# Kernel tuning notes

Hardware: AMD Instinct MI355X
Metric: run time of the kernel (lower is better)

## Reference

```python
import jax, jax.numpy as jnp
import numpy as np

B, N = 4096, 64
H_DIM, U_DIM, Z_DIM, ATTN_DIM, RANK, ALPHA = 256, 128, 16, 64, 4, 1.0
SCALE = ALPHA / float(RANK)  # LowRankDelta scale
LN_EPS = 1e-5


def setup_inputs() -> dict:
    key = jax.random.key(0)
    ks = jax.random.split(key, 12)
    std = 0.02
    return {
        "h": jax.random.normal(ks[0], (B, N, H_DIM), jnp.float32),
        "u": jax.random.normal(ks[1], (B, N, U_DIM), jnp.float32),
        "z": jax.random.normal(ks[2], (B, N, Z_DIM), jnp.float32),
        # LowRankDelta weights (stored as [in, rank] / [rank, out]); up weights
        # are zero-init in torch but randomized here so the math is non-trivial.
        "qd_down": jax.random.normal(ks[3], (H_DIM + Z_DIM, RANK), jnp.float32) * std,
        "qd_up": jax.random.normal(ks[4], (RANK, ATTN_DIM), jnp.float32) * std,
        "kd_down": jax.random.normal(ks[5], (U_DIM, RANK), jnp.float32) * std,
        "kd_up": jax.random.normal(ks[6], (RANK, ATTN_DIM), jnp.float32) * std,
        "vd_down": jax.random.normal(ks[7], (U_DIM, RANK), jnp.float32) * std,
        "vd_up": jax.random.normal(ks[8], (RANK, ATTN_DIM), jnp.float32) * std,
        "od_down": jax.random.normal(ks[9], (ATTN_DIM, RANK), jnp.float32) * std,
        "od_up": jax.random.normal(ks[10], (RANK, U_DIM), jnp.float32) * std,
        # MemeticStateCell: mix_in = z+h+u = 400
        "ug_w": jax.random.normal(ks[11], (Z_DIM + H_DIM + U_DIM, Z_DIM), jnp.float32) * std,
        "ug_b": jnp.zeros((Z_DIM,), jnp.float32),
        "cand_w": jax.random.normal(jax.random.fold_in(key, 99), (Z_DIM + H_DIM + U_DIM, Z_DIM), jnp.float32) * std,
        "cand_b": jnp.zeros((Z_DIM,), jnp.float32),
        "eta_logit": jnp.float32(-1.5),
    }


def _layer_norm(x):
    mu = jnp.mean(x, axis=-1, keepdims=True)
    var = jnp.mean(jnp.square(x - mu), axis=-1, keepdims=True)
    return (x - mu) * jax.lax.rsqrt(var + LN_EPS)


def reference(h, u, z, qd_down, qd_up, kd_down, kd_up, vd_down, vd_up,
              od_down, od_up, ug_w, ug_b, cand_w, cand_b, eta_logit):
    # low-rank q/k/v deltas
    q_in = jnp.concatenate([h, z], axis=-1)                 # [B,N,H+Z]
    q = (q_in @ qd_down) @ qd_up * SCALE                    # [B,N,A]
    k = (u @ kd_down) @ kd_up * SCALE                       # [B,N,A]
    v = (u @ vd_down) @ vd_up * SCALE                       # [B,N,A]

    # masked self-attention over agents
    scores = jnp.einsum('bnd,bmd->bnm', q, k) / jnp.sqrt(jnp.float32(ATTN_DIM))
    eye = jnp.eye(scores.shape[-1], dtype=bool)             # self-mask
    scores = jnp.where(eye, -jnp.inf, scores)
    attn = jax.nn.softmax(scores, axis=-1)                  # [B,N,N]
    c_latent = jnp.einsum('bnm,bmd->bnd', attn, v)          # [B,N,A]
    c = (c_latent @ od_down) @ od_up * SCALE                # [B,N,U]

    # GRU-like gated memetic state update + layernorm
    mix = jnp.concatenate([z, h, c], axis=-1)               # [B,N,Z+H+U]
    gate = jax.nn.sigmoid(mix @ ug_w + ug_b)
    eta = jax.nn.sigmoid(eta_logit)
    proposal = jnp.tanh(mix @ cand_w + cand_b)
    eg = eta * gate
    z_next = _layer_norm((1.0 - eg) * z + eg * proposal)

    return (c, z_next, attn, q, k, v)
```

## Files before the change

### kernel.cpp

```cpp
#include <hip/hip_runtime.h>
#include <math.h>

typedef float v4f __attribute__((ext_vector_type(4)));
typedef short v8s __attribute__((ext_vector_type(8)));

#define NBATCH 4096
#define NT 64
#define HD 256
#define UD 128
#define ZD 16
#define AD 64
#define LRSCALE 0.25f

#define OFF_C    0UL
#define OFF_ZN   33554432UL
#define OFF_ATTN 37748736UL
#define OFF_Q    54525952UL
#define OFF_K    71303168UL
#define OFF_V    88080384UL

#define WS_WT2 13824
#define WS_WOT 15872
#define WS_WCT 24064
#define WS_TOTAL 28160

__device__ __forceinline__ short f2bf(float x) {
  unsigned u = __float_as_uint(x);
  u = (u + 0x7fffu + ((u >> 16) & 1u)) >> 16;
  return (short)u;
}
__device__ __forceinline__ v8s ld8(const short* p) { return *(const v8s*)p; }
__device__ __forceinline__ v8s pack8(v4f x0, v4f x1) {
  v8s a;
  a[0] = f2bf(x0.x); a[1] = f2bf(x0.y); a[2] = f2bf(x0.z); a[3] = f2bf(x0.w);
  a[4] = f2bf(x1.x); a[5] = f2bf(x1.y); a[6] = f2bf(x1.z); a[7] = f2bf(x1.w);
  return a;
}

__global__ void prep_weights(
    const float* __restrict__ qd_down, const float* __restrict__ kd_down,
    const float* __restrict__ vd_down, const float* __restrict__ od_down,
    const float* __restrict__ od_up, const float* __restrict__ ug_w,
    const float* __restrict__ cand_w, short* __restrict__ ws)
{
  int idx = blockIdx.x * 256 + threadIdx.x;
  if (idx < WS_WT2) {
    int n = idx / 288, k = idx - n * 288;
    float val = 0.f;
    if (n < 4) {
      if (k < 272) val = qd_down[k * 4 + n];
    } else if (n >= 16) {
      const float* W = (n < 32) ? ug_w : cand_w;
      int o = (n < 32) ? (n - 16) : (n - 32);
      if (k < 256) val = W[(16 + k) * 16 + o];
      else if (k < 272) val = W[(k - 256) * 16 + o];
    }
    ws[idx] = f2bf(val);
  } else if (idx < WS_WOT) {
    int j = idx - WS_WT2;
    int n = j >> 7, k = j & 127;
    float val = 0.f;
    if (n < 4) val = kd_down[k * 4 + n];
    else if (n < 8) val = vd_down[k * 4 + (n - 4)];
    ws[idx] = f2bf(val);
  } else if (idx < WS_WCT) {
    int j = idx - WS_WOT;
    int e2 = j >> 6, d = j & 63;
    float a = od_down[d * 4 + 0] * od_up[e2] + od_down[d * 4 + 1] * od_up[128 + e2]
            + od_down[d * 4 + 2] * od_up[256 + e2] + od_down[d * 4 + 3] * od_up[384 + e2];
    ws[idx] = f2bf(a * LRSCALE);
  } else if (idx < WS_TOTAL) {
    int j = idx - WS_WCT;
    int o = j >> 7, e2 = j & 127;
    const float* W = (o < 16) ? ug_w : cand_w;
    ws[idx] = f2bf(W[(272 + e2) * 16 + (o & 15)]);
  }
}

__global__ __launch_bounds__(256, 3)
void memetic_fused(
    const float* __restrict__ hg, const float* __restrict__ ug2,
    const float* __restrict__ zg,
    const float* __restrict__ qd_up, const float* __restrict__ kd_up,
    const float* __restrict__ vd_up,
    const float* __restrict__ ug_b, const float* __restrict__ cand_b,
    const float* __restrict__ eta_logit,
    const short* __restrict__ wsw,
    float* __restrict__ c_o, float* __restrict__ zn_o,
    float* __restrict__ attn_o, float* __restrict__ q_o,
    float* __restrict__ k_o, float* __restrict__ v_o)
{
  __shared__ float g1out[NT * 33];
  __shared__ float qkv4[NT * 13];
  __shared__ char scr[36864];

  const int b = blockIdx.x;
  const int tid = threadIdx.x;
  const int lane = tid & 63;
  const int wv = tid >> 6;
  const int quad = lane >> 4;
  const int l16 = lane & 15;

  const short* WT1g = wsw;
  const short* WT2g = wsw + WS_WT2;
  const short* WOTg = wsw + WS_WOT;
  const short* WCTg = wsw + WS_WCT;

  const int tok = wv * 16 + l16;
  const float* hrow = hg + ((size_t)b * NT + tok) * HD;
  const float* urow = ug2 + ((size_t)b * NT + tok) * UD;
  const float* zrow = zg + ((size_t)b * NT + tok) * ZD;

  v4f acc1[3];
  for (int i = 0; i < 3; ++i) acc1[i] = (v4f){0.f, 0.f, 0.f, 0.f};
#pragma unroll
  for (int kc = 0; kc < 9; ++kc) {
    v8s a;
    if (kc < 8) {
      v4f x0 = *(const v4f*)(hrow + kc * 32 + quad * 8);
      v4f x1 = *(const v4f*)(hrow + kc * 32 + quad * 8 + 4);
      a = pack8(x0, x1);
    } else if (quad < 2) {
      v4f x0 = *(const v4f*)(zrow + quad * 8);
      v4f x1 = *(const v4f*)(zrow + quad * 8 + 4);
      a = pack8(x0, x1);
    } else {
      a = (v8s){0, 0, 0, 0, 0, 0, 0, 0};
    }
    const short* wrow = WT1g + kc * 32 + quad * 8;
#pragma unroll
    for (int nt = 0; nt < 3; ++nt) {
      v8s bb = ld8(wrow + (nt * 16 + l16) * 288);
      acc1[nt] = __builtin_amdgcn_mfma_f32_16x16x32_bf16(a, bb, acc1[nt], 0, 0, 0);
    }
  }

  v4f acc2 = (v4f){0.f, 0.f, 0.f, 0.f};
#pragma unroll
  for (int kc = 0; kc < 4; ++kc) {
    v4f x0 = *(const v4f*)(urow + kc * 32 + quad * 8);
    v4f x1 = *(const v4f*)(urow + kc * 32 + quad * 8 + 4);
    v8s a = pack8(x0, x1);
    v8s bb = ld8(WT2g + l16 * 128 + kc * 32 + quad * 8);
    acc2 = __builtin_amdgcn_mfma_f32_16x16x32_bf16(a, bb, acc2, 0, 0, 0);
  }

  if (l16 < 4) {
#pragma unroll
    for (int r = 0; r < 4; ++r)
      qkv4[(wv * 16 + quad * 4 + r) * 13 + l16] = acc1[0][r];
  }
#pragma unroll
  for (int r = 0; r < 4; ++r) {
    int row = wv * 16 + quad * 4 + r;
    g1out[row * 33 + l16] = acc1[1][r];
    g1out[row * 33 + 16 + l16] = acc1[2][r];
  }
  if (l16 < 8) {
#pragma unroll
    for (int r = 0; r < 4; ++r)
      qkv4[(wv * 16 + quad * 4 + r) * 13 + 4 + l16] = acc2[r];
  }
  __syncthreads();

  {
    short* q_s = (short*)scr;
    short* k_s = (short*)(scr + 9216);
    short* vT = (short*)(scr + 18432);
    float qup[4], kup[4], vup[4];
#pragma unroll
    for (int r = 0; r < 4; ++r) {
      qup[r] = qd_up[r * AD + lane];
      kup[r] = kd_up[r * AD + lane];
      vup[r] = vd_up[r * AD + lane];
    }
    for (int i = 0; i < 16; ++i) {
      int t = wv * 16 + i;
      const float* p4 = qkv4 + t * 13;
      float qv = LRSCALE * (p4[0] * qup[0] + p4[1] * qup[1] + p4[2] * qup[2] + p4[3] * qup[3]);
      float kv = LRSCALE * (p4[4] * kup[0] + p4[5] * kup[1] + p4[6] * kup[2] + p4[7] * kup[3]);
      float vv = LRSCALE * (p4[8] * vup[0] + p4[9] * vup[1] + p4[10] * vup[2] + p4[11] * vup[3]);
      size_t go = ((size_t)b * NT + t) * AD + lane;
      q_o[go] = qv; k_o[go] = kv; v_o[go] = vv;
      q_s[t * 72 + lane] = f2bf(qv);
      k_s[t * 72 + lane] = f2bf(kv);
      vT[lane * 72 + t] = f2bf(vv);
    }
  }
  __syncthreads();

  v4f acc3[4];
  for (int i = 0; i < 4; ++i) acc3[i] = (v4f){0.f, 0.f, 0.f, 0.f};
  {
    short* q_s = (short*)scr;
    short* k_s = (short*)(scr + 9216);
#pragma unroll
    for (int kc = 0; kc < 2; ++kc) {
      v8s bb = ld8(k_s + (wv * 16 + l16) * 72 + kc * 32 + quad * 8);
#pragma unroll
      for (int mt = 0; mt < 4; ++mt) {
        v8s a = ld8(q_s + (mt * 16 + l16) * 72 + kc * 32 + quad * 8);
        acc3[mt] = __builtin_amdgcn_mfma_f32_16x16x32_bf16(a, bb, acc3[mt], 0, 0, 0);
      }
    }
  }
  __syncthreads();
  {
    float* attnF = (float*)scr;
#pragma unroll
    for (int mt = 0; mt < 4; ++mt)
#pragma unroll
      for (int r = 0; r < 4; ++r) {
        int row = mt * 16 + quad * 4 + r;
        int col = wv * 16 + l16;
        float s = acc3[mt][r] * 0.125f;
        attnF[row * 66 + col] = (row == col) ? -INFINITY : s;
      }
  }
  __syncthreads();
  {
    float* attnF = (float*)scr;
    short* attnB = (short*)(scr + 27648);
    int n = tid >> 2, p = tid & 3;
    float e[16];
    float mx = -INFINITY;
    const float* rp = attnF + n * 66 + p * 16;
#pragma unroll
    for (int i = 0; i < 16; ++i) { e[i] = rp[i]; mx = fmaxf(mx, e[i]); }
    mx = fmaxf(mx, __shfl_xor(mx, 1));
    mx = fmaxf(mx, __shfl_xor(mx, 2));
    float s = 0.f;
#pragma unroll
    for (int i = 0; i < 16; ++i) { float ee = __expf(e[i] - mx); e[i] = ee; s += ee; }
    s += __shfl_xor(s, 1);
    s += __shfl_xor(s, 2);
    float inv = 1.f / s;
    size_t gb = ((size_t)b * NT + n) * NT + p * 16;
#pragma unroll
    for (int i = 0; i < 16; ++i) {
      float av = e[i] * inv;
      attn_o[gb + i] = av;
      attnB[n * 72 + p * 16 + i] = f2bf(av);
    }
  }
  __syncthreads();

  v4f acc4[4];
  for (int i = 0; i < 4; ++i) acc4[i] = (v4f){0.f, 0.f, 0.f, 0.f};
  {
    short* attnB = (short*)(scr + 27648);
    short* vT = (short*)(scr + 18432);
#pragma unroll
    for (int kc = 0; kc < 2; ++kc) {
      v8s bb = ld8(vT + (wv * 16 + l16) * 72 + kc * 32 + quad * 8);
#pragma unroll
      for (int mt = 0; mt < 4; ++mt) {
        v8s a = ld8(attnB + (mt * 16 + l16) * 72 + kc * 32 + quad * 8);
        acc4[mt] = __builtin_amdgcn_mfma_f32_16x16x32_bf16(a, bb, acc4[mt], 0, 0, 0);
      }
    }
  }
  {
    short* clB = (short*)scr;
#pragma unroll
    for (int mt = 0; mt < 4; ++mt)
#pragma unroll
      for (int r = 0; r < 4; ++r)
        clB[(mt * 16 + quad * 4 + r) * 72 + wv * 16 + l16] = f2bf(acc4[mt][r]);
  }
  __syncthreads();

  v4f acc5[4][2];
  for (int i = 0; i < 4; ++i)
    for (int j = 0; j < 2; ++j) acc5[i][j] = (v4f){0.f, 0.f, 0.f, 0.f};
  {
    short* clB = (short*)scr;
#pragma unroll
    for (int kc = 0; kc < 2; ++kc)
#pragma unroll
      for (int mt = 0; mt < 4; ++mt) {
        v8s a = ld8(clB + (mt * 16 + l16) * 72 + kc * 32 + quad * 8);
#pragma unroll
        for (int j = 0; j < 2; ++j) {
          v8s bb = ld8(WOTg + ((wv + 4 * j) * 16 + l16) * 64 + kc * 32 + quad * 8);
          acc5[mt][j] = __builtin_amdgcn_mfma_f32_16x16x32_bf16(a, bb, acc5[mt][j], 0, 0, 0);
        }
      }
  }
  {
    short* cB = (short*)(scr + 9216);
#pragma unroll
    for (int mt = 0; mt < 4; ++mt)
#pragma unroll
      for (int j = 0; j < 2; ++j)
#pragma unroll
        for (int r = 0; r < 4; ++r) {
          int row = mt * 16 + quad * 4 + r;
          int e2 = (wv + 4 * j) * 16 + l16;
          float val = acc5[mt][j][r];
          c_o[((size_t)b * NT + row) * UD + e2] = val;
          cB[row * 136 + e2] = f2bf(val);
        }
  }
  __syncthreads();

  v4f acc6[2];
  for (int i = 0; i < 2; ++i) acc6[i] = (v4f){0.f, 0.f, 0.f, 0.f};
  {
    short* cB = (short*)(scr + 9216);
#pragma unroll
    for (int kc = 0; kc < 4; ++kc) {
      v8s a = ld8(cB + (wv * 16 + l16) * 136 + kc * 32 + quad * 8);
#pragma unroll
      for (int nt = 0; nt < 2; ++nt) {
        v8s bb = ld8(WCTg + (nt * 16 + l16) * 128 + kc * 32 + quad * 8);
        acc6[nt] = __builtin_amdgcn_mfma_f32_16x16x32_bf16(a, bb, acc6[nt], 0, 0, 0);
      }
    }
  }
#pragma unroll
  for (int nt = 0; nt < 2; ++nt)
#pragma unroll
    for (int r = 0; r < 4; ++r) {
      int row = wv * 16 + quad * 4 + r;
      g1out[row * 33 + nt * 16 + l16] += acc6[nt][r];
    }
  __syncthreads();

  if (tid < NT) {
    const int t = tid;
    const float* zr = zg + ((size_t)b * NT + t) * ZD;
    float eta = 1.f / (1.f + __expf(-eta_logit[0]));
    float x[16];
    float mean = 0.f;
#pragma unroll
    for (int o = 0; o < 16; ++o) {
      float gpre = g1out[t * 33 + o] + ug_b[o];
      float cpre = g1out[t * 33 + 16 + o] + cand_b[o];
      float gate = 1.f / (1.f + __expf(-gpre));
      float prop = tanhf(cpre);
      float eg = eta * gate;
      float xv = (1.f - eg) * zr[o] + eg * prop;
      x[o] = xv;
      mean += xv;
    }
    mean *= (1.f / 16.f);
    float var = 0.f;
#pragma unroll
    for (int o = 0; o < 16; ++o) { float d0 = x[o] - mean; var += d0 * d0; }
    var *= (1.f / 16.f);
    float rs = rsqrtf(var + 1e-5f);
#pragma unroll
    for (int o = 0; o < 16; ++o)
      zn_o[((size_t)b * NT + t) * ZD + o] = (x[o] - mean) * rs;
  }
}

extern "C" void kernel_launch(void* const* d_in, const int* in_sizes, int n_in,
                              void* d_out, int out_size, void* d_ws, size_t ws_size,
                              hipStream_t stream) {
  const float* h = (const float*)d_in[0];
  const float* u = (const float*)d_in[1];
  const float* z = (const float*)d_in[2];
  const float* qd_down = (const float*)d_in[3];
  const float* qd_up = (const float*)d_in[4];
  const float* kd_down = (const float*)d_in[5];
  const float* kd_up = (const float*)d_in[6];
  const float* vd_down = (const float*)d_in[7];
  const float* vd_up = (const float*)d_in[8];
  const float* od_down = (const float*)d_in[9];
  const float* od_up = (const float*)d_in[10];
  const float* ug_w = (const float*)d_in[11];
  const float* ug_b = (const float*)d_in[12];
  const float* cand_w = (const float*)d_in[13];
  const float* cand_b = (const float*)d_in[14];
  const float* eta_logit = (const float*)d_in[15];
  float* out = (float*)d_out;
  short* ws = (short*)d_ws;

  prep_weights<<<(WS_TOTAL + 255) / 256, 256, 0, stream>>>(
      qd_down, kd_down, vd_down, od_down, od_up, ug_w, cand_w, ws);

  memetic_fused<<<NBATCH, 256, 0, stream>>>(
      h, u, z, qd_up, kd_up, vd_up, ug_b, cand_b, eta_logit, ws,
      out + OFF_C, out + OFF_ZN, out + OFF_ATTN,
      out + OFF_Q, out + OFF_K, out + OFF_V);
}
```

Before: 734.8 us.

## Exploit rank-4 structure: compute attention and output projection in low-rank space

Scores are now computed as q4·M4·k4, with a precomputed 4x4 matrix M4 = qd_up·kd_upᵀ, instead of building bf16 Q/K tiles and running MFMA. Attention·V is done on the 4-wide v latents in registers. c and its gate/candidate contribution come from small precomputed rank-4 matrices. This drops several LDS round trips, syncthreads and MFMA stages, cuts LDS use so occupancy can rise to 4 blocks, and swaps the bf16 packing for the hardware v_cvt_pk_bf16_f32 instruction. Scores and the c path now use fp32 with weights fused on device, which changes numerics slightly.

```diff
diff --git a/kernel.cpp b/kernel.cpp
--- a/kernel.cpp
+++ b/kernel.cpp
@@ -19,10 +19,11 @@
 #define OFF_K    71303168UL
 #define OFF_V    88080384UL
 
-#define WS_WT2 13824
-#define WS_WOT 15872
-#define WS_WCT 24064
-#define WS_TOTAL 28160
+#define WS_WT2OFF 13824
+#define WS_SHORTS 15872
+#define F_M4   0
+#define F_C4UP 16
+#define F_G4   528
 
 __device__ __forceinline__ short f2bf(float x) {
   unsigned u = __float_as_uint(x);
@@ -30,54 +31,87 @@
   return (short)u;
 }
 __device__ __forceinline__ v8s ld8(const short* p) { return *(const v8s*)p; }
+
+__device__ __forceinline__ unsigned cvt2(float lo, float hi) {
+  unsigned r;
+  asm("v_cvt_pk_bf16_f32 %0, %1, %2" : "=v"(r) : "v"(lo), "v"(hi));
+  return r;
+}
 __device__ __forceinline__ v8s pack8(v4f x0, v4f x1) {
-  v8s a;
-  a[0] = f2bf(x0.x); a[1] = f2bf(x0.y); a[2] = f2bf(x0.z); a[3] = f2bf(x0.w);
-  a[4] = f2bf(x1.x); a[5] = f2bf(x1.y); a[6] = f2bf(x1.z); a[7] = f2bf(x1.w);
-  return a;
+  union { unsigned u[4]; v8s s; } z;
+  z.u[0] = cvt2(x0.x, x0.y);
+  z.u[1] = cvt2(x0.z, x0.w);
+  z.u[2] = cvt2(x1.x, x1.y);
+  z.u[3] = cvt2(x1.z, x1.w);
+  return z.s;
 }
 
 __global__ void prep_weights(
-    const float* __restrict__ qd_down, const float* __restrict__ kd_down,
-    const float* __restrict__ vd_down, const float* __restrict__ od_down,
-    const float* __restrict__ od_up, const float* __restrict__ ug_w,
-    const float* __restrict__ cand_w, short* __restrict__ ws)
+    const float* __restrict__ qd_down, const float* __restrict__ qd_up,
+    const float* __restrict__ kd_down, const float* __restrict__ kd_up,
+    const float* __restrict__ vd_down, const float* __restrict__ vd_up,
+    const float* __restrict__ od_down, const float* __restrict__ od_up,
+    const float* __restrict__ ug_w, const float* __restrict__ cand_w,
+    short* __restrict__ ws)
 {
-  int idx = blockIdx.x * 256 + threadIdx.x;
-  if (idx < WS_WT2) {
-    int n = idx / 288, k = idx - n * 288;
+  __shared__ float p44s[16];
+  __shared__ float c4up_s[512];
+  const int tid = threadIdx.x;
+
+  for (int idx = blockIdx.x * 256 + tid; idx < WS_SHORTS; idx += 8 * 256) {
     float val = 0.f;
-    if (n < 4) {
-      if (k < 272) val = qd_down[k * 4 + n];
-    } else if (n >= 16) {
-      const float* W = (n < 32) ? ug_w : cand_w;
-      int o = (n < 32) ? (n - 16) : (n - 32);
-      if (k < 256) val = W[(16 + k) * 16 + o];
-      else if (k < 272) val = W[(k - 256) * 16 + o];
+    if (idx < WS_WT2OFF) {
+      int n = idx / 288, k = idx - n * 288;
+      if (n < 4) {
+        if (k < 272) val = qd_down[k * 4 + n];
+      } else if (n >= 16) {
+        const float* W = (n < 32) ? ug_w : cand_w;
+        int o = (n < 32) ? (n - 16) : (n - 32);
+        if (k < 256) val = W[(16 + k) * 16 + o];
+        else if (k < 272) val = W[(k - 256) * 16 + o];
+      }
+    } else {
+      int j = idx - WS_WT2OFF;
+      int n = j >> 7, k = j & 127;
+      if (n < 4) val = kd_down[k * 4 + n];
+      else if (n < 8) val = vd_down[k * 4 + (n - 4)];
     }
     ws[idx] = f2bf(val);
-  } else if (idx < WS_WOT) {
-    int j = idx - WS_WT2;
-    int n = j >> 7, k = j & 127;
-    float val = 0.f;
-    if (n < 4) val = kd_down[k * 4 + n];
-    else if (n < 8) val = vd_down[k * 4 + (n - 4)];
-    ws[idx] = f2bf(val);
-  } else if (idx < WS_WCT) {
-    int j = idx - WS_WOT;
-    int e2 = j >> 6, d = j & 63;
-    float a = od_down[d * 4 + 0] * od_up[e2] + od_down[d * 4 + 1] * od_up[128 + e2]
-            + od_down[d * 4 + 2] * od_up[256 + e2] + od_down[d * 4 + 3] * od_up[384 + e2];
-    ws[idx] = f2bf(a * LRSCALE);
-  } else if (idx < WS_TOTAL) {
-    int j = idx - WS_WCT;
-    int o = j >> 7, e2 = j & 127;
+  }
+
+  if (blockIdx.x != 0) return;
+  float* wsf = (float*)(ws + WS_SHORTS);
+
+  if (tid < 16) {
+    int r = tid >> 2, s = tid & 3;
+    float acc = 0.f;
+    for (int d = 0; d < 64; ++d) acc += qd_up[r * 64 + d] * kd_up[s * 64 + d];
+    wsf[F_M4 + tid] = acc * (LRSCALE * LRSCALE * 0.125f);
+  } else if (tid < 32) {
+    int j = (tid - 16) >> 2, i2 = tid & 3;
+    float acc = 0.f;
+    for (int d = 0; d < 64; ++d) acc += vd_up[j * 64 + d] * od_down[d * 4 + i2];
+    p44s[tid - 16] = acc * (LRSCALE * LRSCALE);
+  }
+  __syncthreads();
+  for (int idx = tid; idx < 512; idx += 256) {
+    int j = idx >> 7, e = idx & 127;
+    float acc = 0.f;
+    for (int i2 = 0; i2 < 4; ++i2) acc += p44s[j * 4 + i2] * od_up[i2 * 128 + e];
+    c4up_s[idx] = acc;
+    wsf[F_C4UP + idx] = acc;
+  }
+  __syncthreads();
+  if (tid < 128) {
+    int j = tid >> 5, o = tid & 31;
     const float* W = (o < 16) ? ug_w : cand_w;
-    ws[idx] = f2bf(W[(272 + e2) * 16 + (o & 15)]);
-  }
-}
-
-__global__ __launch_bounds__(256, 3)
+    float acc = 0.f;
+    for (int e = 0; e < 128; ++e) acc += c4up_s[j * 128 + e] * W[(272 + e) * 16 + (o & 15)];
+    wsf[F_G4 + tid] = acc;
+  }
+}
+
+__global__ __launch_bounds__(256, 4)
 void memetic_fused(
     const float* __restrict__ hg, const float* __restrict__ ug2,
     const float* __restrict__ zg,
@@ -91,8 +125,11 @@
     float* __restrict__ k_o, float* __restrict__ v_o)
 {
   __shared__ float g1out[NT * 33];
-  __shared__ float qkv4[NT * 13];
-  __shared__ char scr[36864];
+  __shared__ float q4s[NT * 4];
+  __shared__ float kv8[NT * 8 + 16];
+  __shared__ float cl4s[NT * 4];
+  __shared__ float c4up_lds[512];
+  __shared__ float g4_lds[128];
 
   const int b = blockIdx.x;
   const int tid = threadIdx.x;
@@ -102,9 +139,12 @@
   const int l16 = lane & 15;
 
   const short* WT1g = wsw;
-  const short* WT2g = wsw + WS_WT2;
-  const short* WOTg = wsw + WS_WOT;
-  const short* WCTg = wsw + WS_WCT;
+  const short* WT2g = wsw + WS_WT2OFF;
+  const float* F32 = (const float*)(wsw + WS_SHORTS);
+
+  c4up_lds[tid] = F32[F_C4UP + tid];
+  c4up_lds[256 + tid] = F32[F_C4UP + 256 + tid];
+  if (tid < 128) g4_lds[tid] = F32[F_G4 + tid];
 
   const int tok = wv * 16 + l16;
   const float* hrow = hg + ((size_t)b * NT + tok) * HD;
@@ -134,7 +174,6 @@
       acc1[nt] = __builtin_amdgcn_mfma_f32_16x16x32_bf16(a, bb, acc1[nt], 0, 0, 0);
     }
   }
-
   v4f acc2 = (v4f){0.f, 0.f, 0.f, 0.f};
 #pragma unroll
   for (int kc = 0; kc < 4; ++kc) {
@@ -148,7 +187,7 @@
   if (l16 < 4) {
 #pragma unroll
     for (int r = 0; r < 4; ++r)
-      qkv4[(wv * 16 + quad * 4 + r) * 13 + l16] = acc1[0][r];
+      q4s[(wv * 16 + quad * 4 + r) * 4 + l16] = acc1[0][r];
   }
 #pragma unroll
   for (int r = 0; r < 4; ++r) {
@@ -158,15 +197,67 @@
   }
   if (l16 < 8) {
 #pragma unroll
-    for (int r = 0; r < 4; ++r)
-      qkv4[(wv * 16 + quad * 4 + r) * 13 + 4 + l16] = acc2[r];
+    for (int r = 0; r < 4; ++r) {
+      int row = wv * 16 + quad * 4 + r;
+      kv8[row * 8 + wv * 4 + l16] = acc2[r];
+    }
   }
   __syncthreads();
 
+  const int n = tid >> 2, p = tid & 3;
   {
-    short* q_s = (short*)scr;
-    short* k_s = (short*)(scr + 9216);
-    short* vT = (short*)(scr + 18432);
+    v4f q4v = *(const v4f*)(q4s + n * 4);
+    float M4v[16];
+#pragma unroll
+    for (int t = 0; t < 16; ++t) M4v[t] = F32[F_M4 + t];
+    float qm[4];
+#pragma unroll
+    for (int s2 = 0; s2 < 4; ++s2)
+      qm[s2] = q4v.x * M4v[s2] + q4v.y * M4v[4 + s2] + q4v.z * M4v[8 + s2] + q4v.w * M4v[12 + s2];
+
+    float e[16];
+    float mx = -INFINITY;
+#pragma unroll
+    for (int i = 0; i < 16; ++i) {
+      int m = p * 16 + i;
+      v4f k4 = *(const v4f*)(kv8 + m * 8 + p * 4);
+      float s = qm[0] * k4.x + qm[1] * k4.y + qm[2] * k4.z + qm[3] * k4.w;
+      e[i] = (m == n) ? -INFINITY : s;
+      mx = fmaxf(mx, e[i]);
+    }
+    mx = fmaxf(mx, __shfl_xor(mx, 1));
+    mx = fmaxf(mx, __shfl_xor(mx, 2));
+    float ssum = 0.f;
+#pragma unroll
+    for (int i = 0; i < 16; ++i) { float ee = __expf(e[i] - mx); e[i] = ee; ssum += ee; }
+    ssum += __shfl_xor(ssum, 1);
+    ssum += __shfl_xor(ssum, 2);
+    float inv = 1.f / ssum;
+
+    v4f cl = (v4f){0.f, 0.f, 0.f, 0.f};
+#pragma unroll
+    for (int i = 0; i < 16; ++i) {
+      float av = e[i] * inv;
+      e[i] = av;
+      int m = p * 16 + i;
+      v4f v4 = *(const v4f*)(kv8 + m * 8 + p * 4 + 4);
+      cl += av * v4;
+    }
+    size_t gb = ((size_t)b * NT + n) * NT + p * 16;
+#pragma unroll
+    for (int i = 0; i < 4; ++i)
+      *(v4f*)(attn_o + gb + i * 4) = (v4f){e[4 * i], e[4 * i + 1], e[4 * i + 2], e[4 * i + 3]};
+#pragma unroll
+    for (int rnd = 1; rnd <= 2; rnd <<= 1) {
+      cl.x += __shfl_xor(cl.x, rnd);
+      cl.y += __shfl_xor(cl.y, rnd);
+      cl.z += __shfl_xor(cl.z, rnd);
+      cl.w += __shfl_xor(cl.w, rnd);
+    }
+    if (p == 0) *(v4f*)(cl4s + n * 4) = cl;
+  }
+
+  {
     float qup[4], kup[4], vup[4];
 #pragma unroll
     for (int r = 0; r < 4; ++r) {
@@ -176,155 +267,38 @@
     }
     for (int i = 0; i < 16; ++i) {
       int t = wv * 16 + i;
-      const float* p4 = qkv4 + t * 13;
-      float qv = LRSCALE * (p4[0] * qup[0] + p4[1] * qup[1] + p4[2] * qup[2] + p4[3] * qup[3]);
-      float kv = LRSCALE * (p4[4] * kup[0] + p4[5] * kup[1] + p4[6] * kup[2] + p4[7] * kup[3]);
-      float vv = LRSCALE * (p4[8] * vup[0] + p4[9] * vup[1] + p4[10] * vup[2] + p4[11] * vup[3]);
+      v4f q4 = *(const v4f*)(q4s + t * 4);
+      const float* kr = kv8 + t * 8 + wv * 4;
+      v4f k4 = *(const v4f*)kr;
+      v4f v4 = *(const v4f*)(kr + 4);
+      float qv = LRSCALE * (q4.x * qup[0] + q4.y * qup[1] + q4.z * qup[2] + q4.w * qup[3]);
+      float kv = LRSCALE * (k4.x * kup[0] + k4.y * kup[1] + k4.z * kup[2] + k4.w * kup[3]);
+      float vv = LRSCALE * (v4.x * vup[0] + v4.y * vup[1] + v4.z * vup[2] + v4.w * vup[3]);
       size_t go = ((size_t)b * NT + t) * AD + lane;
       q_o[go] = qv; k_o[go] = kv; v_o[go] = vv;
-      q_s[t * 72 + lane] = f2bf(qv);
-      k_s[t * 72 + lane] = f2bf(kv);
-      vT[lane * 72 + t] = f2bf(vv);
-    }
-  }
-  __syncthreads();
-
-  v4f acc3[4];
-  for (int i = 0; i < 4; ++i) acc3[i] = (v4f){0.f, 0.f, 0.f, 0.f};
+    }
+  }
+
   {
-    short* q_s = (short*)scr;
-    short* k_s = (short*)(scr + 9216);
-#pragma unroll
-    for (int kc = 0; kc < 2; ++kc) {
-      v8s bb = ld8(k_s + (wv * 16 + l16) * 72 + kc * 32 + quad * 8);
-#pragma unroll
-      for (int mt = 0; mt < 4; ++mt) {
-        v8s a = ld8(q_s + (mt * 16 + l16) * 72 + kc * 32 + quad * 8);
-        acc3[mt] = __builtin_amdgcn_mfma_f32_16x16x32_bf16(a, bb, acc3[mt], 0, 0, 0);
-      }
-    }
-  }
-  __syncthreads();
-  {
-    float* attnF = (float*)scr;
-#pragma unroll
-    for (int mt = 0; mt < 4; ++mt)
-#pragma unroll
-      for (int r = 0; r < 4; ++r) {
-        int row = mt * 16 + quad * 4 + r;
-        int col = wv * 16 + l16;
-        float s = acc3[mt][r] * 0.125f;
-        attnF[row * 66 + col] = (row == col) ? -INFINITY : s;
-      }
-  }
-  __syncthreads();
-  {
-    float* attnF = (float*)scr;
-    short* attnB = (short*)(scr + 27648);
-    int n = tid >> 2, p = tid & 3;
-    float e[16];
-    float mx = -INFINITY;
-    const float* rp = attnF + n * 66 + p * 16;
-#pragma unroll
-    for (int i = 0; i < 16; ++i) { e[i] = rp[i]; mx = fmaxf(mx, e[i]); }
-    mx = fmaxf(mx, __shfl_xor(mx, 1));
-    mx = fmaxf(mx, __shfl_xor(mx, 2));
-    float s = 0.f;
-#pragma unroll
-    for (int i = 0; i < 16; ++i) { float ee = __expf(e[i] - mx); e[i] = ee; s += ee; }
-    s += __shfl_xor(s, 1);
-    s += __shfl_xor(s, 2);
-    float inv = 1.f / s;
-    size_t gb = ((size_t)b * NT + n) * NT + p * 16;
-#pragma unroll
-    for (int i = 0; i < 16; ++i) {
-      float av = e[i] * inv;
-      attn_o[gb + i] = av;
-      attnB[n * 72 + p * 16 + i] = f2bf(av);
-    }
-  }
-  __syncthreads();
-
-  v4f acc4[4];
-  for (int i = 0; i < 4; ++i) acc4[i] = (v4f){0.f, 0.f, 0.f, 0.f};
-  {
-    short* attnB = (short*)(scr + 27648);
-    short* vT = (short*)(scr + 18432);
-#pragma unroll
-    for (int kc = 0; kc < 2; ++kc) {
-      v8s bb = ld8(vT + (wv * 16 + l16) * 72 + kc * 32 + quad * 8);
-#pragma unroll
-      for (int mt = 0; mt < 4; ++mt) {
-        v8s a = ld8(attnB + (mt * 16 + l16) * 72 + kc * 32 + quad * 8);
-        acc4[mt] = __builtin_amdgcn_mfma_f32_16x16x32_bf16(a, bb, acc4[mt], 0, 0, 0);
-      }
-    }
-  }
-  {
-    short* clB = (short*)scr;
-#pragma unroll
-    for (int mt = 0; mt < 4; ++mt)
-#pragma unroll
-      for (int r = 0; r < 4; ++r)
-        clB[(mt * 16 + quad * 4 + r) * 72 + wv * 16 + l16] = f2bf(acc4[mt][r]);
-  }
-  __syncthreads();
-
-  v4f acc5[4][2];
-  for (int i = 0; i < 4; ++i)
-    for (int j = 0; j < 2; ++j) acc5[i][j] = (v4f){0.f, 0.f, 0.f, 0.f};
-  {
-    short* clB = (short*)scr;
-#pragma unroll
-    for (int kc = 0; kc < 2; ++kc)
-#pragma unroll
-      for (int mt = 0; mt < 4; ++mt) {
-        v8s a = ld8(clB + (mt * 16 + l16) * 72 + kc * 32 + quad * 8);
-#pragma unroll
-        for (int j = 0; j < 2; ++j) {
-          v8s bb = ld8(WOTg + ((wv + 4 * j) * 16 + l16) * 64 + kc * 32 + quad * 8);
-          acc5[mt][j] = __builtin_amdgcn_mfma_f32_16x16x32_bf16(a, bb, acc5[mt][j], 0, 0, 0);
-        }
-      }
-  }
-  {
-    short* cB = (short*)(scr + 9216);
-#pragma unroll
-    for (int mt = 0; mt < 4; ++mt)
-#pragma unroll
-      for (int j = 0; j < 2; ++j)
-#pragma unroll
-        for (int r = 0; r < 4; ++r) {
-          int row = mt * 16 + quad * 4 + r;
-          int e2 = (wv + 4 * j) * 16 + l16;
-          float val = acc5[mt][j][r];
-          c_o[((size_t)b * NT + row) * UD + e2] = val;
-          cB[row * 136 + e2] = f2bf(val);
-        }
-  }
-  __syncthreads();
-
-  v4f acc6[2];
-  for (int i = 0; i < 2; ++i) acc6[i] = (v4f){0.f, 0.f, 0.f, 0.f};
-  {
-    short* cB = (short*)(scr + 9216);
-#pragma unroll
-    for (int kc = 0; kc < 4; ++kc) {
-      v8s a = ld8(cB + (wv * 16 + l16) * 136 + kc * 32 + quad * 8);
-#pragma unroll
-      for (int nt = 0; nt < 2; ++nt) {
-        v8s bb = ld8(WCTg + (nt * 16 + l16) * 128 + kc * 32 + quad * 8);
-        acc6[nt] = __builtin_amdgcn_mfma_f32_16x16x32_bf16(a, bb, acc6[nt], 0, 0, 0);
-      }
-    }
-  }
-#pragma unroll
-  for (int nt = 0; nt < 2; ++nt)
-#pragma unroll
-    for (int r = 0; r < 4; ++r) {
-      int row = wv * 16 + quad * 4 + r;
-      g1out[row * 33 + nt * 16 + l16] += acc6[nt][r];
-    }
+    v4f cl = *(const v4f*)(cl4s + n * 4);
+    float* crow = c_o + ((size_t)b * NT + n) * UD;
+#pragma unroll
+    for (int k2 = 0; k2 < 8; ++k2) {
+      int ch = p + 4 * k2;
+      v4f acc = cl.x * *(const v4f*)(c4up_lds + 0 * 128 + ch * 4)
+              + cl.y * *(const v4f*)(c4up_lds + 1 * 128 + ch * 4)
+              + cl.z * *(const v4f*)(c4up_lds + 2 * 128 + ch * 4)
+              + cl.w * *(const v4f*)(c4up_lds + 3 * 128 + ch * 4);
+      *(v4f*)(crow + ch * 4) = acc;
+    }
+#pragma unroll
+    for (int k2 = 0; k2 < 8; ++k2) {
+      int o = p + 4 * k2;
+      float add = cl.x * g4_lds[o] + cl.y * g4_lds[32 + o]
+                + cl.z * g4_lds[64 + o] + cl.w * g4_lds[96 + o];
+      g1out[n * 33 + o] += add;
+    }
+  }
   __syncthreads();
 
   if (tid < NT) {
@@ -378,8 +352,9 @@
   float* out = (float*)d_out;
   short* ws = (short*)d_ws;
 
-  prep_weights<<<(WS_TOTAL + 255) / 256, 256, 0, stream>>>(
-      qd_down, kd_down, vd_down, od_down, od_up, ug_w, cand_w, ws);
+  prep_weights<<<8, 256, 0, stream>>>(
+      qd_down, qd_up, kd_down, kd_up, vd_down, vd_up,
+      od_down, od_up, ug_w, cand_w, ws);
 
   memetic_fused<<<NBATCH, 256, 0, stream>>>(
       h, u, z, qd_up, kd_up, vd_up, ug_b, cand_b, eta_logit, ws,
```

Result: slower. 760.7 us (+3.5%).
